# Kernel optimization log

Measured on AMD Instinct MI355X. Metric: run time of the kernel, lower is better.

## Reference

```python
import jax, jax.numpy as jnp
import numpy as np

NUM_USER = 20000
NUM_ITEM = 20000
N = NUM_USER + NUM_ITEM
E = 250000
DIM_X = 64
NEG_SLOPE = 0.01  # F.leaky_relu default
EPS = 1e-12


def _xavier(key, shape):
    scale = (2.0 / (shape[0] + shape[1])) ** 0.5
    return jax.random.normal(key, shape, dtype=jnp.float32) * scale


def setup_inputs() -> dict:
    key = jax.random.key(0)
    ks = iter(jax.random.split(key, 64))
    inp = {}
    feat_dims = {'v': 2048, 'a': 128, 't': 100}
    lat_dims = {'v': 256, 'a': 128, 't': 100}
    for m in ('v', 'a', 't'):
        Fd, L = feat_dims[m], lat_dims[m]
        inp[m + '_feat'] = jax.random.normal(next(ks), (NUM_ITEM, Fd), dtype=jnp.float32)
        inp[m + '_pref'] = _xavier(next(ks), (NUM_USER, L))
        inp[m + '_mlp_w'] = _xavier(next(ks), (Fd, L))
        inp[m + '_mlp_b'] = jnp.zeros((L,), jnp.float32)
        inp[m + '_conv_w'] = _xavier(next(ks), (L, L))
        inp[m + '_conv_b'] = jnp.zeros((L,), jnp.float32)
        inp[m + '_lin_w'] = _xavier(next(ks), (L, DIM_X))
        inp[m + '_lin_b'] = jnp.zeros((DIM_X,), jnp.float32)
        inp[m + '_g_w'] = _xavier(next(ks), (L, DIM_X))
        inp[m + '_g_b'] = jnp.zeros((DIM_X,), jnp.float32)
    inp['id_emb'] = _xavier(next(ks), (N, DIM_X))
    src = jax.random.randint(next(ks), (E,), 0, NUM_USER)
    dst = jax.random.randint(next(ks), (E,), NUM_USER, N)
    inp['edge_index'] = jnp.stack([src, dst])  # [2, E] user->item
    inp['user_nodes'] = jax.random.randint(next(ks), (1024,), 0, NUM_USER)
    inp['pos_items'] = jax.random.randint(next(ks), (1024,), NUM_USER, N)
    inp['neg_items'] = jax.random.randint(next(ks), (1024,), NUM_USER, N)
    return inp


def _l2norm(x):
    return x / jnp.maximum(jnp.linalg.norm(x, axis=-1, keepdims=True), EPS)


def _graph_gat(x, src, dst, w, b):
    # x: [N, L] -> per-edge gather, gated attention, scatter-add (aggr='add')
    xw = x @ w                      # [N, L]
    x_j = xw[src]                   # source (neighbor) features, [E, L]
    x_i = xw[dst]                   # destination features, [E, L]
    inner = jnp.sum(x_i * x_j, axis=-1)                      # [E]
    deg = jax.ops.segment_sum(jnp.ones_like(inner), src, num_segments=N)
    gate = jax.nn.sigmoid(inner * (deg[src] ** -0.5))        # degree-scaled gate
    logits = inner * gate
    seg_max = jax.ops.segment_max(logits, dst, num_segments=N)
    e = jnp.exp(logits - seg_max[dst])
    denom = jax.ops.segment_sum(e, dst, num_segments=N)
    alpha = e / jnp.maximum(denom[dst], 1e-16)               # softmax over in-edges of dst
    out = jax.ops.segment_sum(x_j * alpha[:, None], dst, num_segments=N)
    return _l2norm(out + b)


def _gnn(feat, pref, mlp_w, mlp_b, conv_w, conv_b, lin_w, lin_b, g_w, g_b, id_emb, src, dst):
    temp = jnp.tanh(feat @ mlp_w + mlp_b)                    # [num_item, L]
    x = _l2norm(jnp.concatenate([pref, temp], axis=0))        # [N, L]
    h = jax.nn.leaky_relu(_graph_gat(x, src, dst, conv_w, conv_b), NEG_SLOPE)
    x_hat = jax.nn.leaky_relu(x @ lin_w + lin_b, NEG_SLOPE) + id_emb
    return jax.nn.leaky_relu(h @ g_w + g_b + x_hat, NEG_SLOPE)  # [N, 64]


def reference(v_feat, a_feat, t_feat,
              v_pref, v_mlp_w, v_mlp_b, v_conv_w, v_conv_b, v_lin_w, v_lin_b, v_g_w, v_g_b,
              a_pref, a_mlp_w, a_mlp_b, a_conv_w, a_conv_b, a_lin_w, a_lin_b, a_g_w, a_g_b,
              t_pref, t_mlp_w, t_mlp_b, t_conv_w, t_conv_b, t_lin_w, t_lin_b, t_g_w, t_g_b,
              id_emb, edge_index, user_nodes, pos_items, neg_items):
    # __init__ doubles the edge list with its reverse (undirected graph)
    ei = jnp.concatenate([edge_index, edge_index[::-1]], axis=1)
    src, dst = ei[0], ei[1]
    v_rep = _gnn(v_feat, v_pref, v_mlp_w, v_mlp_b, v_conv_w, v_conv_b, v_lin_w, v_lin_b, v_g_w, v_g_b, id_emb, src, dst)
    a_rep = _gnn(a_feat, a_pref, a_mlp_w, a_mlp_b, a_conv_w, a_conv_b, a_lin_w, a_lin_b, a_g_w, a_g_b, id_emb, src, dst)
    t_rep = _gnn(t_feat, t_pref, t_mlp_w, t_mlp_b, t_conv_w, t_conv_b, t_lin_w, t_lin_b, t_g_w, t_g_b, id_emb, src, dst)
    rep = (v_rep + a_rep + t_rep) / 3.0                      # [N, 64]
    pos_scores = jnp.sum(rep[user_nodes] * rep[pos_items], axis=1)
    neg_scores = jnp.sum(rep[user_nodes] * rep[neg_items], axis=1)
    return (pos_scores, neg_scores)
```

## Files before the change

### kernel.cpp

```cpp
#include <hip/hip_runtime.h>
#include <math.h>

#define NUSER 20000
#define NITEM 20000
#define NNODE 40000
#define MP_USER 20096
#define MP_NODE 40064

typedef unsigned short u16;
typedef __attribute__((ext_vector_type(8))) short bf16x8;
typedef __attribute__((ext_vector_type(4))) float f32x4;

__device__ __forceinline__ float leaky(float v){ return v > 0.0f ? v : 0.01f*v; }
__device__ __forceinline__ u16 f2bf(float f){
  unsigned u = __float_as_uint(f);
  return (u16)((u + 0x7FFFu + ((u>>16)&1u)) >> 16);
}
__device__ __forceinline__ float bf2f(u16 h){ return __uint_as_float(((unsigned)h)<<16); }
__device__ __forceinline__ unsigned pack2(u16 a, u16 b){ return (unsigned)a | ((unsigned)b<<16); }

enum { EPI_STORE=0, EPI_TANH=1, EPI_LEAKY_ADD=2, EPI_ACCUM=3, EPI_NONE=4 };

template<int WR, int WC, int MI, int EPI, bool ASPLIT, int SPLITK>
__global__ __launch_bounds__(WR*WC*64)
void wgemm_k(const float* __restrict__ A, const u16* __restrict__ Ah, const u16* __restrict__ Al,
             const u16* __restrict__ Bh, const u16* __restrict__ Bl,
             const float* __restrict__ bias, const float* __restrict__ add,
             float* __restrict__ C, int M, int N, int K, int Kp)
{
  constexpr int BM = WR*MI*16, BN = WC*64, T = WR*WC*64, NI = 4;
  __shared__ u16 Ash[4*BM*8], Asl[4*BM*8], Bsh[4*BN*8], Bsl[4*BN*8];
  const int tid = threadIdx.x, lane = tid & 63, wid = tid >> 6;
  const int wrow = wid / WC, wcol = wid % WC;
  const int row0 = blockIdx.y*BM;
  const int fr = lane & 15, kg = lane >> 4;
  const int Kc = Kp / SPLITK;
  const int ks0 = (SPLITK > 1) ? blockIdx.z * Kc : 0;

  f32x4 acc[MI][NI] = {};

  for (int kt = 0; kt < Kc; kt += 32) {
    if (ASPLIT) {
      constexpr int AG = BM*4;
      #pragma unroll
      for (int i = 0; i < 2*AG/T; i++) {
        int g = tid + i*T;
        int gi = (g < AG) ? g : g - AG;
        int r = gi >> 2, kk = gi & 3;
        size_t ofs = (size_t)(row0+r)*Kp + ks0 + kt + kk*8;
        int G = (kk*BM + (r ^ (kk<<1)))*8;
        if (g < AG) *(uint4*)&Ash[G] = *(const uint4*)(Ah + ofs);
        else        *(uint4*)&Asl[G] = *(const uint4*)(Al + ofs);
      }
    } else {
      constexpr int AG = BM*4;
      #pragma unroll
      for (int i = 0; i < AG/T; i++) {
        int g = tid + i*T;
        int r = g >> 2, kk = g & 3;
        int gr = row0 + r, gk = ks0 + kt + kk*8;
        float fv[8];
        if (gr < M && gk + 8 <= K) {
          *(float4*)&fv[0] = *(const float4*)(A + (size_t)gr*K + gk);
          *(float4*)&fv[4] = *(const float4*)(A + (size_t)gr*K + gk + 4);
        } else {
          #pragma unroll
          for (int j=0;j<8;j++) fv[j] = (gr < M && gk + j < K) ? A[(size_t)gr*K + gk + j] : 0.f;
        }
        u16 hs[8], ls[8];
        #pragma unroll
        for (int j=0;j<8;j++){ u16 h = f2bf(fv[j]); hs[j]=h; ls[j]=f2bf(fv[j]-bf2f(h)); }
        int G = (kk*BM + (r ^ (kk<<1)))*8;
        *(uint4*)&Ash[G] = make_uint4(pack2(hs[0],hs[1]),pack2(hs[2],hs[3]),pack2(hs[4],hs[5]),pack2(hs[6],hs[7]));
        *(uint4*)&Asl[G] = make_uint4(pack2(ls[0],ls[1]),pack2(ls[2],ls[3]),pack2(ls[4],ls[5]),pack2(ls[6],ls[7]));
      }
    }
    {
      constexpr int BG = BN*4;
      #pragma unroll
      for (int i = 0; i < 2*BG/T; i++) {
        int g = tid + i*T;
        int gi = (g < BG) ? g : g - BG;
        int r = gi >> 2, kk = gi & 3;
        size_t ofs = (size_t)r*Kp + ks0 + kt + kk*8;
        int G = (kk*BN + (r ^ (kk<<1)))*8;
        if (g < BG) *(uint4*)&Bsh[G] = *(const uint4*)(Bh + ofs);
        else        *(uint4*)&Bsl[G] = *(const uint4*)(Bl + ofs);
      }
    }
    __syncthreads();
    bf16x8 ah_[MI], al_[MI], bh_[NI], bl_[NI];
    #pragma unroll
    for (int mi=0;mi<MI;mi++){
      int rw = wrow*(MI*16) + mi*16 + fr;
      int G = (kg*BM + (rw ^ (kg<<1)))*8;
      ah_[mi] = *(const bf16x8*)&Ash[G];
      al_[mi] = *(const bf16x8*)&Asl[G];
    }
    #pragma unroll
    for (int ni=0;ni<NI;ni++){
      int cw = wcol*64 + ni*16 + fr;
      int G = (kg*BN + (cw ^ (kg<<1)))*8;
      bh_[ni] = *(const bf16x8*)&Bsh[G];
      bl_[ni] = *(const bf16x8*)&Bsl[G];
    }
    #pragma unroll
    for (int mi=0;mi<MI;mi++)
      #pragma unroll
      for (int ni=0;ni<NI;ni++){
        acc[mi][ni] = __builtin_amdgcn_mfma_f32_16x16x32_bf16(ah_[mi], bh_[ni], acc[mi][ni], 0,0,0);
        acc[mi][ni] = __builtin_amdgcn_mfma_f32_16x16x32_bf16(ah_[mi], bl_[ni], acc[mi][ni], 0,0,0);
        acc[mi][ni] = __builtin_amdgcn_mfma_f32_16x16x32_bf16(al_[mi], bh_[ni], acc[mi][ni], 0,0,0);
      }
    __syncthreads();
  }
  float* Cb = (EPI==EPI_NONE) ? (C + (size_t)blockIdx.z*MP_USER*N) : C;
  #pragma unroll
  for (int mi=0;mi<MI;mi++){
    #pragma unroll
    for (int ni=0;ni<NI;ni++){
      int col = wcol*64 + ni*16 + fr;
      if (EPI!=EPI_NONE && col >= N) continue;
      #pragma unroll
      for (int r=0;r<4;r++){
        int row = row0 + wrow*(MI*16) + mi*16 + kg*4 + r;
        if (EPI!=EPI_NONE && row >= M) continue;
        size_t idx = (size_t)row*N + col;
        float v = acc[mi][ni][r];
        if (EPI==EPI_NONE)           Cb[idx] = v;
        else if (EPI==EPI_STORE)     Cb[idx] = v;
        else if (EPI==EPI_TANH)      Cb[idx] = tanhf(v + bias[col]);
        else if (EPI==EPI_LEAKY_ADD) Cb[idx] = leaky(v + bias[col]) + add[idx];
        else                         Cb[idx] += leaky(v + bias[col] + add[idx]);
      }
    }
  }
}

struct WDesc { const float* w; u16 *th, *tl; int K, N, Kp, Np; };
struct WPack { WDesc d[12]; };
__global__ void split_w_k(WPack P)
{
  WDesc D = P.d[blockIdx.y];
  int gid = blockIdx.x*256 + threadIdx.x;
  int tot = D.Np * D.Kp;
  if (gid >= tot) return;
  int k = gid / D.Np, n = gid % D.Np;
  float v = (k < D.K && n < D.N) ? D.w[(size_t)k*D.N + n] : 0.f;
  u16 h = f2bf(v);
  D.th[(size_t)n*D.Kp + k] = h;
  D.tl[(size_t)n*D.Kp + k] = f2bf(v - bf2f(h));
}

__global__ void count_deg(const int* __restrict__ ei, int* __restrict__ deg, int E)
{
  int e = blockIdx.x*blockDim.x + threadIdx.x;
  if (e >= 2*E) return;
  int dst = (e < E) ? ei[e+E] : ei[e-E];
  atomicAdd(&deg[dst], 1);
}

__global__ void scan_rowptr(const int* __restrict__ deg, int* __restrict__ row_ptr, int n)
{
  __shared__ int wsum[4];
  __shared__ int carry;
  int tid = threadIdx.x, lane = tid & 63, wid = tid >> 6;
  if (tid==0) carry = 0;
  __syncthreads();
  for (int base=0; base<n; base+=1024) {
    int i0 = base + tid*4;
    int d[4];
    #pragma unroll
    for (int k=0;k<4;k++) d[k] = (i0+k < n) ? deg[i0+k] : 0;
    int t = d[0]+d[1]+d[2]+d[3];
    int incl = t;
    #pragma unroll
    for (int o=1;o<64;o<<=1){ int v = __shfl_up(incl, o); if (lane >= o) incl += v; }
    if (lane==63) wsum[wid] = incl;
    __syncthreads();
    int pre = carry;
    for (int w=0; w<wid; w++) pre += wsum[w];
    int run = pre + incl - t;
    #pragma unroll
    for (int k=0;k<4;k++){ run += d[k]; if (i0+k < n) row_ptr[i0+k+1] = run; }
    __syncthreads();
    if (tid==0) carry += wsum[0]+wsum[1]+wsum[2]+wsum[3];
  }
  if (tid==0) row_ptr[0] = 0;
}

__global__ void fill_csr(const int* __restrict__ ei, const int* __restrict__ row_ptr,
                         int* __restrict__ row_fill, int* __restrict__ col_src,
                         int* __restrict__ col_dst, int E)
{
  int e = blockIdx.x*blockDim.x + threadIdx.x;
  if (e >= 2*E) return;
  int src = ei[e];
  int dst = (e < E) ? ei[e+E] : ei[e-E];
  int pos = row_ptr[dst] + atomicAdd(&row_fill[dst], 1);
  col_src[pos] = src;
  col_dst[pos] = dst;
}

template<int VW>
__device__ __forceinline__ void loadrow(const float* __restrict__ r, int c0, int L, float* v){
  if (c0 + VW <= L) {
    if (VW==4) *(float4*)v = *(const float4*)r;
    else       *(float2*)v = *(const float2*)r;
  } else {
    #pragma unroll
    for (int j=0;j<VW;j++) v[j] = (c0+j < L) ? r[j] : 0.f;
  }
}

template<int VW>
__global__ __launch_bounds__(256)
void l2norm_split_k(const float* __restrict__ pref, const float* __restrict__ xp,
                    const float* __restrict__ bias,
                    u16* __restrict__ xh, u16* __restrict__ xl, int L, int Kp, int nchunk)
{
  int row = (blockIdx.x*blockDim.x + threadIdx.x) >> 6;
  int lane = threadIdx.x & 63;
  if (row >= MP_NODE) return;
  int c0 = lane*VW;
  size_t ofs = (size_t)row*Kp + c0;
  if (row >= NNODE) {
    if (VW==4) { *(uint2*)&xh[ofs] = make_uint2(0,0); *(uint2*)&xl[ofs] = make_uint2(0,0); }
    else       { *(unsigned*)&xh[ofs] = 0; *(unsigned*)&xl[ofs] = 0; }
    return;
  }
  float v[VW];
  if (row < NUSER) {
    loadrow<VW>(pref + (size_t)row*L + c0, c0, L, v);
  } else {
    int i = row - NUSER;
    size_t po = (size_t)i*Kp + c0;
    float s[VW] = {};
    for (int z = 0; z < nchunk; z++) {
      float a[VW];
      const float* src = xp + (size_t)z*MP_USER*Kp + po;
      if (VW==4) *(float4*)a = *(const float4*)src;
      else       *(float2*)a = *(const float2*)src;
      #pragma unroll
      for (int j=0;j<VW;j++) s[j] += a[j];
    }
    #pragma unroll
    for (int j=0;j<VW;j++){
      int c = c0+j;
      float t = s[j] + ((c<L) ? bias[c] : 0.f);
      v[j] = (c<L) ? tanhf(t) : 0.f;
    }
  }
  float ss = 0.f;
  #pragma unroll
  for (int j=0;j<VW;j++) ss += v[j]*v[j];
  #pragma unroll
  for (int o=32;o;o>>=1) ss += __shfl_xor(ss, o);
  float inv = 1.0f / fmaxf(sqrtf(ss), 1e-12f);
  u16 hs[VW], ls[VW];
  #pragma unroll
  for (int j=0;j<VW;j++){
    float val = (c0+j < L) ? v[j]*inv : 0.f;
    hs[j] = f2bf(val); ls[j] = f2bf(val - bf2f(hs[j]));
  }
  if (VW==4) { *(uint2*)&xh[ofs] = make_uint2(pack2(hs[0],hs[1]),pack2(hs[2],hs[3]));
               *(uint2*)&xl[ofs] = make_uint2(pack2(ls[0],ls[1]),pack2(ls[2],ls[3])); }
  else       { *(unsigned*)&xh[ofs] = pack2(hs[0],hs[1]); *(unsigned*)&xl[ofs] = pack2(ls[0],ls[1]); }
}

__global__ __launch_bounds__(256)
void edge_logits_k(const float* __restrict__ xw, const int* __restrict__ col_src,
                   const int* __restrict__ col_dst, const int* __restrict__ deg,
                   float* __restrict__ logits, int L, int E2)
{
  int p = (blockIdx.x*blockDim.x + threadIdx.x) >> 4;
  int j = threadIdx.x & 15;
  if (p >= E2) return;
  int src = col_src[p], dst = col_dst[p];
  const float* ps = xw + (size_t)src*L;
  const float* pd = xw + (size_t)dst*L;
  float dot = 0.f;
  for (int c = j*4; c < L; c += 64) {
    float4 a = *(const float4*)(ps + c);
    float4 b = *(const float4*)(pd + c);
    dot += a.x*b.x + a.y*b.y + a.z*b.z + a.w*b.w;
  }
  #pragma unroll
  for (int o=8;o;o>>=1) dot += __shfl_xor(dot, o, 16);
  if (j==0) {
    float t = dot / sqrtf((float)deg[src]);
    float gate = 1.0f/(1.0f + expf(-t));
    logits[p] = dot * gate;
  }
}

__global__ __launch_bounds__(256)
void node_softmax(const float* __restrict__ logits, const int* __restrict__ row_ptr,
                  float* __restrict__ alpha, int n)
{
  int node = (blockIdx.x*blockDim.x + threadIdx.x) >> 6;
  int lane = threadIdx.x & 63;
  if (node >= n) return;
  int s = row_ptr[node], e = row_ptr[node+1];
  int cnt = e - s;
  if (cnt == 0) return;
  if (cnt <= 64) {
    float lv = (lane < cnt) ? logits[s+lane] : -INFINITY;
    float m = lv;
    #pragma unroll
    for (int o=32;o;o>>=1) m = fmaxf(m, __shfl_xor(m, o));
    float el = (lane < cnt) ? expf(lv - m) : 0.f;
    float d = el;
    #pragma unroll
    for (int o=32;o;o>>=1) d += __shfl_xor(d, o);
    if (lane < cnt) alpha[s+lane] = el / fmaxf(d, 1e-16f);
  } else {
    float m = -INFINITY;
    for (int q=s+lane;q<e;q+=64) m = fmaxf(m, logits[q]);
    #pragma unroll
    for (int o=32;o;o>>=1) m = fmaxf(m, __shfl_xor(m, o));
    float d = 0.f;
    for (int q=s+lane;q<e;q+=64) d += expf(logits[q]-m);
    #pragma unroll
    for (int o=32;o;o>>=1) d += __shfl_xor(d, o);
    float inv = 1.0f / fmaxf(d, 1e-16f);
    for (int q=s+lane;q<e;q+=64) alpha[q] = expf(logits[q]-m)*inv;
  }
}

template<int VW>
__global__ __launch_bounds__(256)
void aggregate_k(const float* __restrict__ xw, const float* __restrict__ alpha,
                 const int* __restrict__ row_ptr, const int* __restrict__ col_src,
                 const float* __restrict__ bias, u16* __restrict__ hh, u16* __restrict__ hl,
                 int L, int Kp)
{
  int node = (blockIdx.x*blockDim.x + threadIdx.x) >> 6;
  int lane = threadIdx.x & 63;
  if (node >= MP_NODE) return;
  int c0 = lane*VW;
  size_t ofs = (size_t)node*Kp + c0;
  if (node >= NNODE) {
    if (VW==4) { *(uint2*)&hh[ofs] = make_uint2(0,0); *(uint2*)&hl[ofs] = make_uint2(0,0); }
    else       { *(unsigned*)&hh[ofs] = 0; *(unsigned*)&hl[ofs] = 0; }
    return;
  }
  float acc[VW] = {};
  int s = row_ptr[node], e = row_ptr[node+1];
  for (int p=s;p<e;p++) {
    float a = alpha[p];
    float v[VW];
    loadrow<VW>(xw + (size_t)col_src[p]*L + c0, c0, L, v);
    #pragma unroll
    for (int j=0;j<VW;j++) acc[j] = fmaf(a, v[j], acc[j]);
  }
  float t[VW], ss = 0.f;
  #pragma unroll
  for (int j=0;j<VW;j++){ int c = c0+j; t[j] = (c<L) ? acc[j]+bias[c] : 0.f; ss += t[j]*t[j]; }
  #pragma unroll
  for (int o=32;o;o>>=1) ss += __shfl_xor(ss, o);
  float inv = 1.0f / fmaxf(sqrtf(ss), 1e-12f);
  u16 hs[VW], ls[VW];
  #pragma unroll
  for (int j=0;j<VW;j++){
    float o2 = (c0+j < L) ? leaky(t[j]*inv) : 0.f;
    hs[j] = f2bf(o2); ls[j] = f2bf(o2 - bf2f(hs[j]));
  }
  if (VW==4) { *(uint2*)&hh[ofs] = make_uint2(pack2(hs[0],hs[1]),pack2(hs[2],hs[3]));
               *(uint2*)&hl[ofs] = make_uint2(pack2(ls[0],ls[1]),pack2(ls[2],ls[3])); }
  else       { *(unsigned*)&hh[ofs] = pack2(hs[0],hs[1]); *(unsigned*)&hl[ofs] = pack2(ls[0],ls[1]); }
}

__global__ __launch_bounds__(256)
void score_k(const float* __restrict__ rep, const int* __restrict__ un,
             const int* __restrict__ pi, const int* __restrict__ ni, float* __restrict__ out)
{
  int wid = (blockIdx.x*blockDim.x + threadIdx.x) >> 6;
  int lane = threadIdx.x & 63;
  if (wid >= 2048) return;
  int i = wid & 1023;
  int isneg = wid >> 10;
  int u = un[i];
  int it = isneg ? ni[i] : pi[i];
  float p = rep[(size_t)u*64 + lane] * rep[(size_t)it*64 + lane];
  #pragma unroll
  for (int o=32;o;o>>=1) p += __shfl_xor(p, o);
  if (lane==0) out[isneg*1024 + i] = p * (1.0f/9.0f);
}

static inline size_t align_up(size_t v){ return (v + 255) & ~(size_t)255; }
static inline int cdiv(int a, int b){ return (a + b - 1) / b; }

extern "C" void kernel_launch(void* const* d_in, const int* in_sizes, int n_in,
                              void* d_out, int out_size, void* d_ws, size_t ws_size,
                              hipStream_t stream)
{
  const int E  = in_sizes[31] / 2;
  const int E2 = 2*E;

  char* p = (char*)d_ws;
  auto carve = [&](size_t bytes){ char* r = p; p += align_up(bytes); return r; };
  float* xw     = (float*)carve((size_t)4*MP_USER*256*4);
  float* xp     = xw;
  u16*   xh     = (u16*)carve((size_t)MP_NODE*256*2);
  u16*   xl     = (u16*)carve((size_t)MP_NODE*256*2);
  float* xhat   = (float*)carve((size_t)NNODE*64*4);
  float* rep    = (float*)carve((size_t)NNODE*64*4);
  float* logits = (float*)carve((size_t)E2*4);
  float* alpha  = (float*)carve((size_t)E2*4);
  int* deg      = (int*)carve((size_t)NNODE*4);
  int* row_ptr  = (int*)carve((size_t)(NNODE+1)*4);
  int* row_fill = (int*)carve((size_t)NNODE*4);
  int* col_src  = (int*)carve((size_t)E2*4);
  int* col_dst  = (int*)carve((size_t)E2*4);

  const int* ei = (const int*)d_in[31];
  const float* id_emb = (const float*)d_in[30];

  struct Mod { const float *feat,*pref,*mlp_w,*mlp_b,*conv_w,*conv_b,*lin_w,*lin_b,*g_w,*g_b;
               int Fd, L, Kpx, Kpf, NpL; };
  Mod md[3];
  for (int m=0;m<3;m++) {
    int b = m*10;
    md[m].feat   = (const float*)d_in[b+0];
    md[m].pref   = (const float*)d_in[b+1];
    md[m].mlp_w  = (const float*)d_in[b+2];
    md[m].mlp_b  = (const float*)d_in[b+3];
    md[m].conv_w = (const float*)d_in[b+4];
    md[m].conv_b = (const float*)d_in[b+5];
    md[m].lin_w  = (const float*)d_in[b+6];
    md[m].lin_b  = (const float*)d_in[b+7];
    md[m].g_w    = (const float*)d_in[b+8];
    md[m].g_b    = (const float*)d_in[b+9];
  }
  md[0].Fd=2048; md[0].L=256; md[0].Kpx=256; md[0].Kpf=2048; md[0].NpL=256;
  md[1].Fd=128;  md[1].L=128; md[1].Kpx=128; md[1].Kpf=128;  md[1].NpL=128;
  md[2].Fd=100;  md[2].L=100; md[2].Kpx=128; md[2].Kpf=128;  md[2].NpL=128;

  u16 *wmh[3],*wml[3],*wch[3],*wcl[3],*wlh[3],*wll[3],*wgh[3],*wgl[3];
  WPack P;
  int maxTot = 0;
  for (int m=0;m<3;m++) {
    const Mod& M_ = md[m];
    size_t smlp = (size_t)M_.NpL*M_.Kpf*2, sconv = (size_t)M_.NpL*M_.Kpx*2, slin = (size_t)64*M_.Kpx*2;
    wmh[m]=(u16*)carve(smlp); wml[m]=(u16*)carve(smlp);
    wch[m]=(u16*)carve(sconv); wcl[m]=(u16*)carve(sconv);
    wlh[m]=(u16*)carve(slin);  wll[m]=(u16*)carve(slin);
    wgh[m]=(u16*)carve(slin);  wgl[m]=(u16*)carve(slin);
    P.d[m*4+0] = { M_.mlp_w,  wmh[m], wml[m], M_.Fd, M_.L, M_.Kpf, M_.NpL };
    P.d[m*4+1] = { M_.conv_w, wch[m], wcl[m], M_.L,  M_.L, M_.Kpx, M_.NpL };
    P.d[m*4+2] = { M_.lin_w,  wlh[m], wll[m], M_.L,  64,   M_.Kpx, 64 };
    P.d[m*4+3] = { M_.g_w,    wgh[m], wgl[m], M_.L,  64,   M_.Kpx, 64 };
    for (int q=0;q<4;q++){ int t = P.d[m*4+q].Np*P.d[m*4+q].Kp; if (t>maxTot) maxTot=t; }
  }

  hipMemsetAsync(deg, 0, (size_t)NNODE*4, stream);
  hipMemsetAsync(row_fill, 0, (size_t)NNODE*4, stream);
  hipMemsetAsync(rep, 0, (size_t)NNODE*64*4, stream);

  { dim3 g(cdiv(maxTot,256), 12); split_w_k<<<g,256,0,stream>>>(P); }
  {
    int blocks = cdiv(E2, 256);
    count_deg<<<blocks,256,0,stream>>>(ei, deg, E);
    scan_rowptr<<<1,256,0,stream>>>(deg, row_ptr, NNODE);
    fill_csr<<<blocks,256,0,stream>>>(ei, row_ptr, row_fill, col_src, col_dst, E);
  }

  for (int m=0;m<3;m++) {
    const Mod& M_ = md[m];
    const int L = M_.L;

    if (m == 0)
      wgemm_k<1,4,4,EPI_NONE,false,4><<<dim3(1,MP_USER/64,4),256,0,stream>>>(
          M_.feat, nullptr, nullptr, wmh[m], wml[m], nullptr, nullptr,
          xp, NUSER, 256, M_.Fd, M_.Kpf);
    else
      wgemm_k<1,2,4,EPI_NONE,false,2><<<dim3(1,MP_USER/64,2),128,0,stream>>>(
          M_.feat, nullptr, nullptr, wmh[m], wml[m], nullptr, nullptr,
          xp, NUSER, 128, M_.Fd, M_.Kpf);

    {
      int nchunk = (m==0) ? 4 : 2;
      if (M_.Kpx==256) l2norm_split_k<4><<<MP_NODE/4,256,0,stream>>>(M_.pref, xp, M_.mlp_b, xh, xl, L, M_.Kpx, nchunk);
      else             l2norm_split_k<2><<<MP_NODE/4,256,0,stream>>>(M_.pref, xp, M_.mlp_b, xh, xl, L, M_.Kpx, nchunk);
    }

    if (m == 0)
      wgemm_k<1,4,4,EPI_STORE,true,1><<<dim3(1,MP_NODE/64,1),256,0,stream>>>(
          nullptr, xh, xl, wch[m], wcl[m], nullptr, nullptr, xw, NNODE, L, L, M_.Kpx);
    else
      wgemm_k<1,2,4,EPI_STORE,true,1><<<dim3(1,MP_NODE/64,1),128,0,stream>>>(
          nullptr, xh, xl, wch[m], wcl[m], nullptr, nullptr, xw, NNODE, L, L, M_.Kpx);

    wgemm_k<4,1,2,EPI_LEAKY_ADD,true,1><<<dim3(1,MP_NODE/128,1),256,0,stream>>>(
        nullptr, xh, xl, wlh[m], wll[m], M_.lin_b, id_emb, xhat, NNODE, 64, L, M_.Kpx);

    edge_logits_k<<<cdiv(E2*16,256),256,0,stream>>>(xw, col_src, col_dst, deg, logits, L, E2);
    node_softmax<<<cdiv(NNODE*64,256),256,0,stream>>>(logits, row_ptr, alpha, NNODE);
    if (M_.Kpx==256) aggregate_k<4><<<MP_NODE/4,256,0,stream>>>(xw, alpha, row_ptr, col_src, M_.conv_b, xh, xl, L, M_.Kpx);
    else             aggregate_k<2><<<MP_NODE/4,256,0,stream>>>(xw, alpha, row_ptr, col_src, M_.conv_b, xh, xl, L, M_.Kpx);

    wgemm_k<4,1,2,EPI_ACCUM,true,1><<<dim3(1,MP_NODE/128,1),256,0,stream>>>(
        nullptr, xh, xl, wgh[m], wgl[m], M_.g_b, xhat, rep, NNODE, 64, L, M_.Kpx);
  }

  score_k<<<cdiv(2048*64,256),256,0,stream>>>(rep, (const int*)d_in[32], (const int*)d_in[33],
                                              (const int*)d_in[34], (float*)d_out);
}
```

Measured before the change: 1.166 ms.

## Double-buffer GEMM shared tiles with direct global-to-LDS async loads

Shared-memory A and B tiles become double-buffered, so the next k-slice is fetched while MFMAs run on the current one. Pre-split bf16 operands are copied with global_load_lds (direct global-to-LDS DMA) instead of going through registers. For fp32 A, the loads are issued early and the bf16 hi/lo conversion is written after the MFMAs. This doubles LDS use and raises register pressure from the held fp32 values, which may lower occupancy.

Result: slower. 1.258 ms (+7.9%).

```diff
diff --git a/kernel.cpp b/kernel.cpp
--- a/kernel.cpp
+++ b/kernel.cpp
@@ -18,6 +18,11 @@
 }
 __device__ __forceinline__ float bf2f(u16 h){ return __uint_as_float(((unsigned)h)<<16); }
 __device__ __forceinline__ unsigned pack2(u16 a, u16 b){ return (unsigned)a | ((unsigned)b<<16); }
+
+__device__ __forceinline__ void gll16(const u16* g, u16* l) {
+  __builtin_amdgcn_global_load_lds((const __attribute__((address_space(1))) void*)g,
+                                   (__attribute__((address_space(3))) void*)l, 16, 0, 0);
+}
 
 enum { EPI_STORE=0, EPI_TANH=1, EPI_LEAKY_ADD=2, EPI_ACCUM=3, EPI_NONE=4 };
 
@@ -29,7 +34,13 @@
              float* __restrict__ C, int M, int N, int K, int Kp)
 {
   constexpr int BM = WR*MI*16, BN = WC*64, T = WR*WC*64, NI = 4;
-  __shared__ u16 Ash[4*BM*8], Asl[4*BM*8], Bsh[4*BN*8], Bsl[4*BN*8];
+  constexpr int AG = BM*4, BG = BN*4;
+  constexpr int AITF = AG/T;
+  constexpr int AIT2 = 2*AG/T;
+  constexpr int BIT2 = 2*BG/T;
+  constexpr int LBM = (BM==64)?6:7;
+  constexpr int LBN = (BN==64)?6:((BN==128)?7:8);
+  __shared__ u16 Ash[2][4*BM*8], Asl[2][4*BM*8], Bsh[2][4*BN*8], Bsl[2][4*BN*8];
   const int tid = threadIdx.x, lane = tid & 63, wid = tid >> 6;
   const int wrow = wid / WC, wcol = wid % WC;
   const int row0 = blockIdx.y*BM;
@@ -39,70 +50,94 @@
 
   f32x4 acc[MI][NI] = {};
 
+#define ASTAGE_GLL(KT, NB) do { \
+  _Pragma("unroll") \
+  for (int i_ = 0; i_ < AIT2; i_++) { \
+    int gb_ = i_*T + wid*64; \
+    bool hi_ = gb_ < AG; \
+    int gl_ = gb_ + lane; \
+    int gi_ = hi_ ? gl_ : gl_ - AG; \
+    int q_ = gi_ & (BM-1), kk_ = gi_ >> LBM; \
+    int r_ = q_ ^ (kk_<<1); \
+    const u16* s_ = (hi_ ? Ah : Al) + (size_t)(row0+r_)*Kp + ks0 + (KT) + kk_*8; \
+    u16* d_ = hi_ ? &Ash[NB][(gb_)*8] : &Asl[NB][(gb_-AG)*8]; \
+    gll16(s_, d_); \
+  } } while(0)
+
+#define BSTAGE_GLL(KT, NB) do { \
+  _Pragma("unroll") \
+  for (int i_ = 0; i_ < BIT2; i_++) { \
+    int gb_ = i_*T + wid*64; \
+    bool hi_ = gb_ < BG; \
+    int gl_ = gb_ + lane; \
+    int gi_ = hi_ ? gl_ : gl_ - BG; \
+    int q_ = gi_ & (BN-1), kk_ = gi_ >> LBN; \
+    int r_ = q_ ^ (kk_<<1); \
+    const u16* s_ = (hi_ ? Bh : Bl) + (size_t)r_*Kp + ks0 + (KT) + kk_*8; \
+    u16* d_ = hi_ ? &Bsh[NB][(gb_)*8] : &Bsl[NB][(gb_-BG)*8]; \
+    gll16(s_, d_); \
+  } } while(0)
+
+#define ALOADF(KT) do { \
+  _Pragma("unroll") \
+  for (int i_ = 0; i_ < AITF; i_++) { \
+    int g_ = tid + i_*T; \
+    int r_ = g_ >> 2, kk_ = g_ & 3; \
+    int gr_ = row0 + r_, gk_ = ks0 + (KT) + kk_*8; \
+    if (gr_ < M && gk_ + 8 <= K) { \
+      *(float4*)&fv[i_][0] = *(const float4*)(A + (size_t)gr_*K + gk_); \
+      *(float4*)&fv[i_][4] = *(const float4*)(A + (size_t)gr_*K + gk_ + 4); \
+    } else { \
+      _Pragma("unroll") \
+      for (int j_=0;j_<8;j_++) fv[i_][j_] = (gr_ < M && gk_ + j_ < K) ? A[(size_t)gr_*K + gk_ + j_] : 0.f; \
+    } \
+  } } while(0)
+
+#define ACONVW(NB) do { \
+  _Pragma("unroll") \
+  for (int i_ = 0; i_ < AITF; i_++) { \
+    int g_ = tid + i_*T; \
+    int r_ = g_ >> 2, kk_ = g_ & 3; \
+    u16 hs_[8], ls_[8]; \
+    _Pragma("unroll") \
+    for (int j_=0;j_<8;j_++){ u16 h_ = f2bf(fv[i_][j_]); hs_[j_]=h_; ls_[j_]=f2bf(fv[i_][j_]-bf2f(h_)); } \
+    int G_ = (kk_*BM + (r_ ^ (kk_<<1)))*8; \
+    *(uint4*)&Ash[NB][G_] = make_uint4(pack2(hs_[0],hs_[1]),pack2(hs_[2],hs_[3]),pack2(hs_[4],hs_[5]),pack2(hs_[6],hs_[7])); \
+    *(uint4*)&Asl[NB][G_] = make_uint4(pack2(ls_[0],ls_[1]),pack2(ls_[2],ls_[3]),pack2(ls_[4],ls_[5]),pack2(ls_[6],ls_[7])); \
+  } } while(0)
+
+  {
+    float fv[AITF][8];
+    if (ASPLIT) { ASTAGE_GLL(0, 0); }
+    else        { ALOADF(0); ACONVW(0); }
+    BSTAGE_GLL(0, 0);
+  }
+  __syncthreads();
+
+  int cur = 0;
   for (int kt = 0; kt < Kc; kt += 32) {
-    if (ASPLIT) {
-      constexpr int AG = BM*4;
-      #pragma unroll
-      for (int i = 0; i < 2*AG/T; i++) {
-        int g = tid + i*T;
-        int gi = (g < AG) ? g : g - AG;
-        int r = gi >> 2, kk = gi & 3;
-        size_t ofs = (size_t)(row0+r)*Kp + ks0 + kt + kk*8;
-        int G = (kk*BM + (r ^ (kk<<1)))*8;
-        if (g < AG) *(uint4*)&Ash[G] = *(const uint4*)(Ah + ofs);
-        else        *(uint4*)&Asl[G] = *(const uint4*)(Al + ofs);
-      }
-    } else {
-      constexpr int AG = BM*4;
-      #pragma unroll
-      for (int i = 0; i < AG/T; i++) {
-        int g = tid + i*T;
-        int r = g >> 2, kk = g & 3;
-        int gr = row0 + r, gk = ks0 + kt + kk*8;
-        float fv[8];
-        if (gr < M && gk + 8 <= K) {
-          *(float4*)&fv[0] = *(const float4*)(A + (size_t)gr*K + gk);
-          *(float4*)&fv[4] = *(const float4*)(A + (size_t)gr*K + gk + 4);
-        } else {
-          #pragma unroll
-          for (int j=0;j<8;j++) fv[j] = (gr < M && gk + j < K) ? A[(size_t)gr*K + gk + j] : 0.f;
-        }
-        u16 hs[8], ls[8];
-        #pragma unroll
-        for (int j=0;j<8;j++){ u16 h = f2bf(fv[j]); hs[j]=h; ls[j]=f2bf(fv[j]-bf2f(h)); }
-        int G = (kk*BM + (r ^ (kk<<1)))*8;
-        *(uint4*)&Ash[G] = make_uint4(pack2(hs[0],hs[1]),pack2(hs[2],hs[3]),pack2(hs[4],hs[5]),pack2(hs[6],hs[7]));
-        *(uint4*)&Asl[G] = make_uint4(pack2(ls[0],ls[1]),pack2(ls[2],ls[3]),pack2(ls[4],ls[5]),pack2(ls[6],ls[7]));
-      }
-    }
-    {
-      constexpr int BG = BN*4;
-      #pragma unroll
-      for (int i = 0; i < 2*BG/T; i++) {
-        int g = tid + i*T;
-        int gi = (g < BG) ? g : g - BG;
-        int r = gi >> 2, kk = gi & 3;
-        size_t ofs = (size_t)r*Kp + ks0 + kt + kk*8;
-        int G = (kk*BN + (r ^ (kk<<1)))*8;
-        if (g < BG) *(uint4*)&Bsh[G] = *(const uint4*)(Bh + ofs);
-        else        *(uint4*)&Bsl[G] = *(const uint4*)(Bl + ofs);
-      }
-    }
-    __syncthreads();
+    const int nb = cur ^ 1;
+    const bool havenext = (kt + 32 < Kc);
+    float fv[AITF][8];
+    if (havenext) {
+      if (ASPLIT) { ASTAGE_GLL(kt+32, nb); }
+      else        { ALOADF(kt+32); }
+      BSTAGE_GLL(kt+32, nb);
+    }
     bf16x8 ah_[MI], al_[MI], bh_[NI], bl_[NI];
     #pragma unroll
     for (int mi=0;mi<MI;mi++){
       int rw = wrow*(MI*16) + mi*16 + fr;
       int G = (kg*BM + (rw ^ (kg<<1)))*8;
-      ah_[mi] = *(const bf16x8*)&Ash[G];
-      al_[mi] = *(const bf16x8*)&Asl[G];
+      ah_[mi] = *(const bf16x8*)&Ash[cur][G];
+      al_[mi] = *(const bf16x8*)&Asl[cur][G];
     }
     #pragma unroll
     for (int ni=0;ni<NI;ni++){
       int cw = wcol*64 + ni*16 + fr;
       int G = (kg*BN + (cw ^ (kg<<1)))*8;
-      bh_[ni] = *(const bf16x8*)&Bsh[G];
-      bl_[ni] = *(const bf16x8*)&Bsl[G];
+      bh_[ni] = *(const bf16x8*)&Bsh[cur][G];
+      bl_[ni] = *(const bf16x8*)&Bsl[cur][G];
     }
     #pragma unroll
     for (int mi=0;mi<MI;mi++)
@@ -112,8 +147,15 @@
         acc[mi][ni] = __builtin_amdgcn_mfma_f32_16x16x32_bf16(ah_[mi], bl_[ni], acc[mi][ni], 0,0,0);
         acc[mi][ni] = __builtin_amdgcn_mfma_f32_16x16x32_bf16(al_[mi], bh_[ni], acc[mi][ni], 0,0,0);
       }
+    if (!ASPLIT && havenext) { ACONVW(nb); }
     __syncthreads();
-  }
+    cur = nb;
+  }
+#undef ASTAGE_GLL
+#undef BSTAGE_GLL
+#undef ALOADF
+#undef ACONVW
+
   float* Cb = (EPI==EPI_NONE) ? (C + (size_t)blockIdx.z*MP_USER*N) : C;
   #pragma unroll
   for (int mi=0;mi<MI;mi++){
```

## Fuse edge logits, per-node softmax and aggregation into one kernel with LDS row cache

Applied to the files above, without the earlier changes.

Replaces the three per-modality edge kernels (edge logits, node softmax, aggregation) with a single per-node wavefront kernel that computes gated logits, does the softmax in registers, and aggregates the neighbor rows. Neighbor rows loaded for the dot product are cached in shared memory (up to CAP per node) so the aggregation pass reuses them instead of re-gathering from global memory. The col_dst and alpha buffers are dropped. The large per-block shared-memory footprint (about 48KB for the 256-wide modality) may limit occupancy, and high-degree nodes still fall back to global logits and reloads.

New measurement: 1.243 ms. 1.07x slower.

```diff
diff --git a/kernel.cpp b/kernel.cpp
--- a/kernel.cpp
+++ b/kernel.cpp
@@ -190,8 +190,7 @@
 }
 
 __global__ void fill_csr(const int* __restrict__ ei, const int* __restrict__ row_ptr,
-                         int* __restrict__ row_fill, int* __restrict__ col_src,
-                         int* __restrict__ col_dst, int E)
+                         int* __restrict__ row_fill, int* __restrict__ col_src, int E)
 {
   int e = blockIdx.x*blockDim.x + threadIdx.x;
   if (e >= 2*E) return;
@@ -199,7 +198,6 @@
   int dst = (e < E) ? ei[e+E] : ei[e-E];
   int pos = row_ptr[dst] + atomicAdd(&row_fill[dst], 1);
   col_src[pos] = src;
-  col_dst[pos] = dst;
 }
 
 template<int VW>
@@ -268,103 +266,125 @@
   else       { *(unsigned*)&xh[ofs] = pack2(hs[0],hs[1]); *(unsigned*)&xl[ofs] = pack2(ls[0],ls[1]); }
 }
 
+template<int VW, int CAP, int LP>
 __global__ __launch_bounds__(256)
-void edge_logits_k(const float* __restrict__ xw, const int* __restrict__ col_src,
-                   const int* __restrict__ col_dst, const int* __restrict__ deg,
-                   float* __restrict__ logits, int L, int E2)
-{
-  int p = (blockIdx.x*blockDim.x + threadIdx.x) >> 4;
-  int j = threadIdx.x & 15;
-  if (p >= E2) return;
-  int src = col_src[p], dst = col_dst[p];
-  const float* ps = xw + (size_t)src*L;
-  const float* pd = xw + (size_t)dst*L;
-  float dot = 0.f;
-  for (int c = j*4; c < L; c += 64) {
-    float4 a = *(const float4*)(ps + c);
-    float4 b = *(const float4*)(pd + c);
-    dot += a.x*b.x + a.y*b.y + a.z*b.z + a.w*b.w;
-  }
-  #pragma unroll
-  for (int o=8;o;o>>=1) dot += __shfl_xor(dot, o, 16);
-  if (j==0) {
-    float t = dot / sqrtf((float)deg[src]);
-    float gate = 1.0f/(1.0f + expf(-t));
-    logits[p] = dot * gate;
-  }
-}
-
-__global__ __launch_bounds__(256)
-void node_softmax(const float* __restrict__ logits, const int* __restrict__ row_ptr,
-                  float* __restrict__ alpha, int n)
-{
-  int node = (blockIdx.x*blockDim.x + threadIdx.x) >> 6;
-  int lane = threadIdx.x & 63;
-  if (node >= n) return;
-  int s = row_ptr[node], e = row_ptr[node+1];
-  int cnt = e - s;
-  if (cnt == 0) return;
-  if (cnt <= 64) {
-    float lv = (lane < cnt) ? logits[s+lane] : -INFINITY;
-    float m = lv;
-    #pragma unroll
-    for (int o=32;o;o>>=1) m = fmaxf(m, __shfl_xor(m, o));
-    float el = (lane < cnt) ? expf(lv - m) : 0.f;
-    float d = el;
-    #pragma unroll
-    for (int o=32;o;o>>=1) d += __shfl_xor(d, o);
-    if (lane < cnt) alpha[s+lane] = el / fmaxf(d, 1e-16f);
-  } else {
-    float m = -INFINITY;
-    for (int q=s+lane;q<e;q+=64) m = fmaxf(m, logits[q]);
-    #pragma unroll
-    for (int o=32;o;o>>=1) m = fmaxf(m, __shfl_xor(m, o));
-    float d = 0.f;
-    for (int q=s+lane;q<e;q+=64) d += expf(logits[q]-m);
-    #pragma unroll
-    for (int o=32;o;o>>=1) d += __shfl_xor(d, o);
-    float inv = 1.0f / fmaxf(d, 1e-16f);
-    for (int q=s+lane;q<e;q+=64) alpha[q] = expf(logits[q]-m)*inv;
-  }
-}
-
-template<int VW>
-__global__ __launch_bounds__(256)
-void aggregate_k(const float* __restrict__ xw, const float* __restrict__ alpha,
-                 const int* __restrict__ row_ptr, const int* __restrict__ col_src,
-                 const float* __restrict__ bias, u16* __restrict__ hh, u16* __restrict__ hl,
-                 int L, int Kp)
-{
-  int node = (blockIdx.x*blockDim.x + threadIdx.x) >> 6;
-  int lane = threadIdx.x & 63;
+void fused_edge_k(const float* __restrict__ xw, const int* __restrict__ row_ptr,
+                  const int* __restrict__ col_src, const int* __restrict__ deg_,
+                  const float* __restrict__ bias, float* __restrict__ glogits,
+                  u16* __restrict__ hh, u16* __restrict__ hl, int L, int Kp)
+{
+  constexpr int KCH = (LP + 63)/64;
+  __shared__ float cache[4][CAP][LP];
+  __shared__ float lsl[4][64];
+  const int slot = threadIdx.x >> 6;
+  const int lane = threadIdx.x & 63;
+  const int node = blockIdx.x*4 + slot;
   if (node >= MP_NODE) return;
-  int c0 = lane*VW;
-  size_t ofs = (size_t)node*Kp + c0;
+  const int c0 = lane*VW;
+  const size_t ofs = (size_t)node*Kp + c0;
   if (node >= NNODE) {
     if (VW==4) { *(uint2*)&hh[ofs] = make_uint2(0,0); *(uint2*)&hl[ofs] = make_uint2(0,0); }
     else       { *(unsigned*)&hh[ofs] = 0; *(unsigned*)&hl[ofs] = 0; }
     return;
   }
+  const int s = row_ptr[node], e = row_ptr[node+1];
+  const int cnt = e - s;
+  const int sw = lane >> 4, j = lane & 15;
+  const bool big = (cnt > 64);
+
+  const float* pd = xw + (size_t)node*L;
+  float4 pdv[KCH];
+  #pragma unroll
+  for (int k=0;k<KCH;k++){
+    int c = j*4 + k*64;
+    pdv[k] = (c < L) ? *(const float4*)(pd + c) : make_float4(0.f,0.f,0.f,0.f);
+  }
+
+  int nit = (cnt + 3) >> 2;
+  for (int it = 0; it < nit; it++) {
+    int i = it*4 + sw;
+    float dot = 0.f;
+    int src = 0;
+    if (i < cnt) {
+      src = col_src[s+i];
+      const float* ps = xw + (size_t)src*L;
+      #pragma unroll
+      for (int k=0;k<KCH;k++){
+        int c = j*4 + k*64;
+        if (c < L) {
+          float4 a = *(const float4*)(ps + c);
+          if (i < CAP) *(float4*)&cache[slot][i][c] = a;
+          dot += a.x*pdv[k].x + a.y*pdv[k].y + a.z*pdv[k].z + a.w*pdv[k].w;
+        }
+      }
+    }
+    #pragma unroll
+    for (int o=8;o;o>>=1) dot += __shfl_xor(dot, o, 16);
+    if (i < cnt && j == 0) {
+      float t = dot / sqrtf((float)deg_[src]);
+      float gate = 1.0f/(1.0f + expf(-t));
+      float lg = dot * gate;
+      if (i < 64) lsl[slot][i] = lg;
+      if (big) glogits[s+i] = lg;
+    }
+  }
+  asm volatile("s_waitcnt lgkmcnt(0)" ::: "memory");
+
+  float alpha_r = 0.f, mxv = 0.f, sinv = 0.f;
+  if (!big) {
+    if (cnt > 0) {
+      float lv = (lane < cnt) ? lsl[slot][lane] : -INFINITY;
+      float m = lv;
+      #pragma unroll
+      for (int o=32;o;o>>=1) m = fmaxf(m, __shfl_xor(m, o));
+      float el = (lane < cnt) ? expf(lv - m) : 0.f;
+      float d = el;
+      #pragma unroll
+      for (int o=32;o;o>>=1) d += __shfl_xor(d, o);
+      alpha_r = el / fmaxf(d, 1e-16f);
+    }
+  } else {
+    asm volatile("s_waitcnt vmcnt(0)" ::: "memory");
+    float m = -INFINITY;
+    for (int q=s+lane;q<e;q+=64) m = fmaxf(m, glogits[q]);
+    #pragma unroll
+    for (int o=32;o;o>>=1) m = fmaxf(m, __shfl_xor(m, o));
+    float d = 0.f;
+    for (int q=s+lane;q<e;q+=64) d += expf(glogits[q]-m);
+    #pragma unroll
+    for (int o=32;o;o>>=1) d += __shfl_xor(d, o);
+    mxv = m; sinv = 1.0f/fmaxf(d, 1e-16f);
+  }
+
   float acc[VW] = {};
-  int s = row_ptr[node], e = row_ptr[node+1];
-  for (int p=s;p<e;p++) {
-    float a = alpha[p];
+  for (int i = 0; i < cnt; i++) {
+    float a = big ? (expf(glogits[s+i]-mxv)*sinv) : __shfl(alpha_r, i);
     float v[VW];
-    loadrow<VW>(xw + (size_t)col_src[p]*L + c0, c0, L, v);
-    #pragma unroll
-    for (int j=0;j<VW;j++) acc[j] = fmaf(a, v[j], acc[j]);
+    if (i < CAP) {
+      if (c0 + VW <= L) {
+        if (VW==4) *(float4*)v = *(const float4*)&cache[slot][i][c0];
+        else       *(float2*)v = *(const float2*)&cache[slot][i][c0];
+      } else {
+        #pragma unroll
+        for (int jj=0;jj<VW;jj++) v[jj] = (c0+jj < L) ? cache[slot][i][c0+jj] : 0.f;
+      }
+    } else {
+      loadrow<VW>(xw + (size_t)col_src[s+i]*L + c0, c0, L, v);
+    }
+    #pragma unroll
+    for (int jj=0;jj<VW;jj++) acc[jj] = fmaf(a, v[jj], acc[jj]);
   }
   float t[VW], ss = 0.f;
   #pragma unroll
-  for (int j=0;j<VW;j++){ int c = c0+j; t[j] = (c<L) ? acc[j]+bias[c] : 0.f; ss += t[j]*t[j]; }
+  for (int jj=0;jj<VW;jj++){ int c = c0+jj; t[jj] = (c<L) ? acc[jj]+bias[c] : 0.f; ss += t[jj]*t[jj]; }
   #pragma unroll
   for (int o=32;o;o>>=1) ss += __shfl_xor(ss, o);
   float inv = 1.0f / fmaxf(sqrtf(ss), 1e-12f);
   u16 hs[VW], ls[VW];
   #pragma unroll
-  for (int j=0;j<VW;j++){
-    float o2 = (c0+j < L) ? leaky(t[j]*inv) : 0.f;
-    hs[j] = f2bf(o2); ls[j] = f2bf(o2 - bf2f(hs[j]));
+  for (int jj=0;jj<VW;jj++){
+    float o2 = (c0+jj < L) ? leaky(t[jj]*inv) : 0.f;
+    hs[jj] = f2bf(o2); ls[jj] = f2bf(o2 - bf2f(hs[jj]));
   }
   if (VW==4) { *(uint2*)&hh[ofs] = make_uint2(pack2(hs[0],hs[1]),pack2(hs[2],hs[3]));
                *(uint2*)&hl[ofs] = make_uint2(pack2(ls[0],ls[1]),pack2(ls[2],ls[3])); }
@@ -407,12 +427,10 @@
   float* xhat   = (float*)carve((size_t)NNODE*64*4);
   float* rep    = (float*)carve((size_t)NNODE*64*4);
   float* logits = (float*)carve((size_t)E2*4);
-  float* alpha  = (float*)carve((size_t)E2*4);
   int* deg      = (int*)carve((size_t)NNODE*4);
   int* row_ptr  = (int*)carve((size_t)(NNODE+1)*4);
   int* row_fill = (int*)carve((size_t)NNODE*4);
   int* col_src  = (int*)carve((size_t)E2*4);
-  int* col_dst  = (int*)carve((size_t)E2*4);
 
   const int* ei = (const int*)d_in[31];
   const float* id_emb = (const float*)d_in[30];
@@ -463,7 +481,7 @@
     int blocks = cdiv(E2, 256);
     count_deg<<<blocks,256,0,stream>>>(ei, deg, E);
     scan_rowptr<<<1,256,0,stream>>>(deg, row_ptr, NNODE);
-    fill_csr<<<blocks,256,0,stream>>>(ei, row_ptr, row_fill, col_src, col_dst, E);
+    fill_csr<<<blocks,256,0,stream>>>(ei, row_ptr, row_fill, col_src, E);
   }
 
   for (int m=0;m<3;m++) {
@@ -495,10 +513,12 @@
     wgemm_k<4,1,2,EPI_LEAKY_ADD,true,1><<<dim3(1,MP_NODE/128,1),256,0,stream>>>(
         nullptr, xh, xl, wlh[m], wll[m], M_.lin_b, id_emb, xhat, NNODE, 64, L, M_.Kpx);
 
-    edge_logits_k<<<cdiv(E2*16,256),256,0,stream>>>(xw, col_src, col_dst, deg, logits, L, E2);
-    node_softmax<<<cdiv(NNODE*64,256),256,0,stream>>>(logits, row_ptr, alpha, NNODE);
-    if (M_.Kpx==256) aggregate_k<4><<<MP_NODE/4,256,0,stream>>>(xw, alpha, row_ptr, col_src, M_.conv_b, xh, xl, L, M_.Kpx);
-    else             aggregate_k<2><<<MP_NODE/4,256,0,stream>>>(xw, alpha, row_ptr, col_src, M_.conv_b, xh, xl, L, M_.Kpx);
+    if (m == 0)
+      fused_edge_k<4,12,256><<<MP_NODE/4,256,0,stream>>>(xw, row_ptr, col_src, deg, M_.conv_b, logits, xh, xl, L, M_.Kpx);
+    else if (m == 1)
+      fused_edge_k<2,20,128><<<MP_NODE/4,256,0,stream>>>(xw, row_ptr, col_src, deg, M_.conv_b, logits, xh, xl, L, M_.Kpx);
+    else
+      fused_edge_k<2,20,104><<<MP_NODE/4,256,0,stream>>>(xw, row_ptr, col_src, deg, M_.conv_b, logits, xh, xl, L, M_.Kpx);
 
     wgemm_k<4,1,2,EPI_ACCUM,true,1><<<dim3(1,MP_NODE/128,1),256,0,stream>>>(
         nullptr, xh, xl, wgh[m], wgl[m], M_.g_b, xhat, rep, NNODE, 64, L, M_.Kpx);
```
